# Kernel tuning notes

Hardware: AMD Instinct MI355X
Metric: run time of the kernel (lower is better)

Reference implementation:

```python
import jax, jax.numpy as jnp
import numpy as np

EPS = 1e-3  # BatchNorm eps from module

def _bn(x, g, b, m, v):
    # torch BatchNorm1d (eval): (x - mean) / sqrt(var + eps) * weight + bias
    return (x - m) * (g / jnp.sqrt(v + EPS)) + b

def setup_inputs() -> dict:
    key = jax.random.key(0)
    ks = jax.random.split(key, 16)
    N, Cin, Cout, S = 1_000_000, 16, 64, 20_000
    inputs = jax.random.normal(ks[0], (N, Cin), dtype=jnp.float32)
    unq_inv = jax.random.randint(ks[1], (N,), 0, S, dtype=jnp.int32)

    def bn_params(k, c):
        k1, k2, k3, k4 = jax.random.split(k, 4)
        return (1.0 + 0.01 * jax.random.normal(k1, (c,), jnp.float32),
                0.01 * jax.random.normal(k2, (c,), jnp.float32),
                0.01 * jax.random.normal(k3, (c,), jnp.float32),
                jax.random.uniform(k4, (c,), jnp.float32, 0.5, 1.5))

    W1 = 0.1 * jax.random.normal(ks[2], (Cin, Cout), jnp.float32)
    g1, b1, m1, v1 = bn_params(ks[3], Cout)
    W2a = 0.1 * jax.random.normal(ks[4], (Cin, 2 * Cout), jnp.float32)
    g2a, b2a, m2a, v2a = bn_params(ks[5], 2 * Cout)
    W2b = 0.1 * jax.random.normal(ks[6], (2 * Cout, Cout), jnp.float32)
    g2b, b2b, m2b, v2b = bn_params(ks[7], Cout)

    return dict(inputs=inputs, unq_inv=unq_inv, num_segments=S,
                W1=W1, g1=g1, b1=b1, m1=m1, v1=v1,
                W2a=W2a, g2a=g2a, b2a=b2a, m2a=m2a, v2a=v2a,
                W2b=W2b, g2b=b2b * 0 + g2b, b2b=b2b, m2b=m2b, v2b=v2b)

def reference(inputs, unq_inv, num_segments,
              W1, g1, b1, m1, v1,
              W2a, g2a, b2a, m2a, v2a,
              W2b, g2b, b2b, m2b, v2b):
    # branch 1: Linear -> BN -> ReLU
    x = jax.nn.relu(_bn(inputs @ W1, g1, b1, m1, v1))            # [N, C]
    # branch 2: Linear -> BN -> ReLU -> Linear -> BN -> ReLU
    h = jax.nn.relu(_bn(inputs @ W2a, g2a, b2a, m2a, v2a))       # [N, 2C]
    x2 = jax.nn.relu(_bn(h @ W2b, g2b, b2b, m2b, v2b))           # [N, C]

    # segment reductions over group ids
    x_max = jax.ops.segment_max(x, unq_inv, num_segments=num_segments)  # [S, C]
    x_max = jnp.maximum(x_max, 0.0)  # empty segments -> 0 (x >= 0 post-ReLU)
    group_sum = jax.ops.segment_sum(x, unq_inv, num_segments=num_segments)  # [S, C]
    max_pool = jnp.max(x2, axis=0)                                # [C], global pool
    max_pool = jnp.broadcast_to(max_pool[None, :], x_max.shape)   # [S, C]

    feat = jnp.concatenate((group_sum, x_max, max_pool), axis=1)  # [S, 3C]
    # channel shuffle with groups=3
    S_, C3 = feat.shape
    feat = feat.reshape(S_, 3, C3 // 3).transpose(0, 2, 1).reshape(S_, C3)
    return feat
```

## Files before the change

### kernel.cpp

```cpp
#include <hip/hip_runtime.h>

#define EPS 1e-3f

#define OFF_T2B    7168
#define OFF_MPP    7232
#define OFF_MPF    11328
#define OFF_CNT    11392
#define OFF_OFFS   31408
#define OFF_CUR    51424
#define OFF_INPS   71424

typedef short short8 __attribute__((ext_vector_type(8)));
typedef float f32x4 __attribute__((ext_vector_type(4)));

union U4 { unsigned u[4]; short8 s8; uint4 u4; };

__device__ inline unsigned short f2bf(float f) {
    unsigned u = __float_as_uint(f);
    return (unsigned short)((u + 0x7FFFu + ((u >> 16) & 1u)) >> 16);
}

__global__ __launch_bounds__(256) void init_k(
    const float* __restrict__ W1,
    const float* __restrict__ g1, const float* __restrict__ b1,
    const float* __restrict__ m1, const float* __restrict__ v1,
    const float* __restrict__ W2a,
    const float* __restrict__ g2a, const float* __restrict__ b2a,
    const float* __restrict__ m2a, const float* __restrict__ v2a,
    const float* __restrict__ W2b,
    const float* __restrict__ g2b, const float* __restrict__ b2b,
    const float* __restrict__ m2b, const float* __restrict__ v2b,
    unsigned short* __restrict__ wsu, float* __restrict__ wsf,
    const int* __restrict__ unq, int* __restrict__ cnt, int N)
{
    const int t = threadIdx.x;
    if (blockIdx.x == 0) {
        for (int i = t; i < 2048; i += 256) {
            int mt = i >> 9, lane = (i >> 3) & 63, j = i & 7;
            int c = lane & 15, g = lane >> 4;
            int k = g * 8 + j, ch = mt * 16 + c;
            float s = g1[ch] * rsqrtf(v1[ch] + EPS);
            float val = (k < 16) ? W1[k * 64 + ch] * s
                      : (k == 16 ? b1[ch] - m1[ch] * s : 0.f);
            wsu[i] = f2bf(val);
        }
        for (int i = t; i < 4096; i += 256) {
            int mt = i >> 9, lane = (i >> 3) & 63, j = i & 7;
            int c = lane & 15, g = lane >> 4;
            int k = g * 8 + j, ch = mt * 16 + c;
            float s = g2a[ch] * rsqrtf(v2a[ch] + EPS);
            float val = (k < 16) ? W2a[k * 128 + ch] * s
                      : (k == 16 ? b2a[ch] - m2a[ch] * s : 0.f);
            wsu[2048 + i] = f2bf(val);
        }
        for (int i = t; i < 8192; i += 256) {
            int f = i >> 9, lane = (i >> 3) & 63, j = i & 7;
            int mt = f >> 2, ks = f & 3;
            int c = lane & 15, g = lane >> 4;
            int k = ks * 32 + g * 8 + j, ch = mt * 16 + c;
            float s = g2b[ch] * rsqrtf(v2b[ch] + EPS);
            wsu[6144 + i] = f2bf(W2b[k * 64 + ch] * s);
        }
        if (t < 64) {
            float s = g2b[t] * rsqrtf(v2b[t] + EPS);
            wsf[OFF_T2B + t] = b2b[t] - m2b[t] * s;
        }
    } else {
        const int i = (blockIdx.x - 1) * 256 + t;
        if (i < N) atomicAdd(&cnt[unq[i]], 1);
    }
}

__global__ __launch_bounds__(1024) void scan_k(
    const int* __restrict__ cnt, int* __restrict__ offs,
    int* __restrict__ cur, int S)
{
    __shared__ int tot[1024];
    const int t = threadIdx.x;
    const int E = (S + 1023) >> 10;
    const int i0 = t * E;
    int run = 0;
    for (int j = 0; j < E; ++j) {
        const int i = i0 + j;
        run += (i < S) ? cnt[i] : 0;
    }
    tot[t] = run;
    __syncthreads();
    for (int d = 1; d < 1024; d <<= 1) {
        int x = (t >= d) ? tot[t - d] : 0;
        __syncthreads();
        tot[t] += x;
        __syncthreads();
    }
    int base = (t == 0) ? 0 : tot[t - 1];
    for (int j = 0; j < E; ++j) {
        const int i = i0 + j;
        if (i < S) {
            offs[i] = base;
            cur[i]  = base;
            base += cnt[i];
        }
    }
    if (t == 1023) offs[S] = tot[1023];
}

__device__ __forceinline__ void b2_tile(
    const U4& bf, bool act, const short8 (&w2a)[8],
    const char* __restrict__ w2bs, char* __restrict__ scr,
    float (&mp)[16], int lane, int c, int g)
{
    const f32x4 zero4 = {0.f, 0.f, 0.f, 0.f};
    __builtin_amdgcn_wave_barrier();
    #pragma unroll
    for (int mt = 0; mt < 8; ++mt) {
        f32x4 hT = __builtin_amdgcn_mfma_f32_16x16x32_bf16(w2a[mt], bf.s8, zero4, 0, 0, 0);
        float h0 = fmaxf(hT[0], 0.f), h1 = fmaxf(hT[1], 0.f);
        float h2 = fmaxf(hT[2], 0.f), h3 = fmaxf(hT[3], 0.f);
        unsigned lo, hi;
        asm("v_cvt_pk_bf16_f32 %0, %1, %2" : "=v"(lo) : "v"(h0), "v"(h1));
        asm("v_cvt_pk_bf16_f32 %0, %1, %2" : "=v"(hi) : "v"(h2), "v"(h3));
        const int gw = 2 * (mt & 1) + (g >> 1);
        *reinterpret_cast<uint2*>(
            &scr[(mt >> 1) * 1024 + (gw * 16 + c) * 16 + (g & 1) * 8])
            = make_uint2(lo, hi);
    }
    __builtin_amdgcn_wave_barrier();
    f32x4 y2t[4];
    #pragma unroll
    for (int mt = 0; mt < 4; ++mt) y2t[mt] = zero4;
    #pragma unroll
    for (int ks = 0; ks < 4; ++ks) {
        short8 hb = *reinterpret_cast<const short8*>(&scr[ks * 1024 + lane * 16]);
        #pragma unroll
        for (int mt = 0; mt < 4; ++mt) {
            short8 a = *reinterpret_cast<const short8*>(
                &w2bs[((mt * 4 + ks) * 64 + lane) * 16]);
            y2t[mt] = __builtin_amdgcn_mfma_f32_16x16x32_bf16(a, hb, y2t[mt], 0, 0, 0);
        }
    }
    #pragma unroll
    for (int mt = 0; mt < 4; ++mt) {
        #pragma unroll
        for (int r = 0; r < 4; ++r)
            mp[mt * 4 + r] = act ? fmaxf(mp[mt * 4 + r], y2t[mt][r]) : mp[mt * 4 + r];
    }
}

__global__ __launch_bounds__(256, 4) void br2_k(
    const float* __restrict__ inputs,
    const uint4* __restrict__ wsw,
    const float* __restrict__ wsf,
    float* __restrict__ mpp,
    int N)
{
    __shared__ __align__(16) char w2bs[16384];
    __shared__ __align__(16) char scrs[4][4096];
    __shared__ float mpb[64];

    const int tid  = threadIdx.x;
    const int wv   = tid >> 6;
    const int lane = tid & 63;
    const int c = lane & 15;
    const int g = lane >> 4;

    #pragma unroll
    for (int u = 0; u < 4; ++u)
        reinterpret_cast<uint4*>(w2bs)[u * 256 + tid] = wsw[768 + u * 256 + tid];
    if (tid < 64) mpb[tid] = 0.f;
    __syncthreads();

    short8 w2a[8];
    #pragma unroll
    for (int s = 0; s < 8; ++s) {
        U4 t; t.u4 = wsw[256 + s * 64 + lane]; w2a[s] = t.s8;
    }
    #pragma unroll
    for (int s = 0; s < 8; ++s) asm volatile("" : "+v"(w2a[s]));

    char* scr = scrs[wv];
    float mp[16];
    #pragma unroll
    for (int j = 0; j < 16; ++j) mp[j] = -3.0e38f;

    const long stride = (long)gridDim.x * 256;
    for (long base = (long)blockIdx.x * 256 + (long)wv * 64; base < N; base += stride) {
        const long nrem = (long)N - base;
        if (nrem >= 64) {
            float4 f0[4], f1[4];
            if (g < 2) {
                const float* ip = inputs + (base + c) * 16 + g * 8;
                #pragma unroll
                for (int ti = 0; ti < 4; ++ti) {
                    const float4* p = reinterpret_cast<const float4*>(ip + ti * 256);
                    f0[ti] = p[0]; f1[ti] = p[1];
                }
            }
            #pragma unroll
            for (int ti = 0; ti < 4; ++ti) {
                U4 bf;
                if (g < 2) {
                    asm("v_cvt_pk_bf16_f32 %0, %1, %2" : "=v"(bf.u[0]) : "v"(f0[ti].x), "v"(f0[ti].y));
                    asm("v_cvt_pk_bf16_f32 %0, %1, %2" : "=v"(bf.u[1]) : "v"(f0[ti].z), "v"(f0[ti].w));
                    asm("v_cvt_pk_bf16_f32 %0, %1, %2" : "=v"(bf.u[2]) : "v"(f1[ti].x), "v"(f1[ti].y));
                    asm("v_cvt_pk_bf16_f32 %0, %1, %2" : "=v"(bf.u[3]) : "v"(f1[ti].z), "v"(f1[ti].w));
                } else {
                    bf.u[0] = (g == 2) ? 0x00003F80u : 0u;
                    bf.u[1] = 0u; bf.u[2] = 0u; bf.u[3] = 0u;
                }
                b2_tile(bf, true, w2a, w2bs, scr, mp, lane, c, g);
            }
        } else {
            #pragma unroll
            for (int ti = 0; ti < 4; ++ti) {
                if ((long)ti * 16 >= nrem) break;
                const bool act = (long)(ti * 16 + c) < nrem;
                U4 bf;
                if (g < 2) {
                    const long row = act ? (base + ti * 16 + c) : (long)(N - 1);
                    const float4* p = reinterpret_cast<const float4*>(inputs + row * 16 + g * 8);
                    float4 q0 = p[0], q1 = p[1];
                    asm("v_cvt_pk_bf16_f32 %0, %1, %2" : "=v"(bf.u[0]) : "v"(q0.x), "v"(q0.y));
                    asm("v_cvt_pk_bf16_f32 %0, %1, %2" : "=v"(bf.u[1]) : "v"(q0.z), "v"(q0.w));
                    asm("v_cvt_pk_bf16_f32 %0, %1, %2" : "=v"(bf.u[2]) : "v"(q1.x), "v"(q1.y));
                    asm("v_cvt_pk_bf16_f32 %0, %1, %2" : "=v"(bf.u[3]) : "v"(q1.z), "v"(q1.w));
                    if (!act) { bf.u[0] = 0u; bf.u[1] = 0u; bf.u[2] = 0u; bf.u[3] = 0u; }
                } else {
                    bf.u[0] = (g == 2 && act) ? 0x00003F80u : 0u;
                    bf.u[1] = 0u; bf.u[2] = 0u; bf.u[3] = 0u;
                }
                b2_tile(bf, act, w2a, w2bs, scr, mp, lane, c, g);
            }
        }
    }

    #pragma unroll
    for (int j = 0; j < 16; ++j) {
        float x = mp[j];
        x = fmaxf(x, __shfl_xor(x, 1, 64));
        x = fmaxf(x, __shfl_xor(x, 2, 64));
        x = fmaxf(x, __shfl_xor(x, 4, 64));
        x = fmaxf(x, __shfl_xor(x, 8, 64));
        mp[j] = x;
    }
    if (c == 0) {
        #pragma unroll
        for (int mt = 0; mt < 4; ++mt)
            #pragma unroll
            for (int r = 0; r < 4; ++r) {
                const int ch = mt * 16 + g * 4 + r;
                const float v = fmaxf(mp[mt * 4 + r] + wsf[OFF_T2B + ch], 0.f);
                atomicMax(reinterpret_cast<int*>(&mpb[ch]), __float_as_int(v));
            }
    }
    __syncthreads();
    if (tid < 64)
        atomicMax(reinterpret_cast<int*>(mpp + (blockIdx.x & 63) * 64 + tid),
                  __float_as_int(mpb[tid]));
}

__global__ __launch_bounds__(256) void scat_k(
    const float* __restrict__ inputs,
    const int*   __restrict__ unq,
    int*         __restrict__ cur,
    uint4*       __restrict__ inpS,
    int N)
{
    const int i = blockIdx.x * 256 + threadIdx.x;
    if (i >= N) return;
    const int seg = unq[i];
    const int pos = atomicAdd(&cur[seg], 1);

    const float4* p = reinterpret_cast<const float4*>(inputs + (size_t)i * 16);
    float4 a0 = p[0], a1 = p[1], a2 = p[2], a3 = p[3];
    unsigned pk[8];
    asm("v_cvt_pk_bf16_f32 %0, %1, %2" : "=v"(pk[0]) : "v"(a0.x), "v"(a0.y));
    asm("v_cvt_pk_bf16_f32 %0, %1, %2" : "=v"(pk[1]) : "v"(a0.z), "v"(a0.w));
    asm("v_cvt_pk_bf16_f32 %0, %1, %2" : "=v"(pk[2]) : "v"(a1.x), "v"(a1.y));
    asm("v_cvt_pk_bf16_f32 %0, %1, %2" : "=v"(pk[3]) : "v"(a1.z), "v"(a1.w));
    asm("v_cvt_pk_bf16_f32 %0, %1, %2" : "=v"(pk[4]) : "v"(a2.x), "v"(a2.y));
    asm("v_cvt_pk_bf16_f32 %0, %1, %2" : "=v"(pk[5]) : "v"(a2.z), "v"(a2.w));
    asm("v_cvt_pk_bf16_f32 %0, %1, %2" : "=v"(pk[6]) : "v"(a3.x), "v"(a3.y));
    asm("v_cvt_pk_bf16_f32 %0, %1, %2" : "=v"(pk[7]) : "v"(a3.z), "v"(a3.w));

    inpS[(size_t)pos * 2]     = make_uint4(pk[0], pk[1], pk[2], pk[3]);
    inpS[(size_t)pos * 2 + 1] = make_uint4(pk[4], pk[5], pk[6], pk[7]);
}

__global__ __launch_bounds__(64) void fin_k(
    const float* __restrict__ mpp, float* __restrict__ mpf)
{
    const int t = threadIdx.x;
    float m = 0.f;
    #pragma unroll
    for (int s = 0; s < 64; ++s)
        m = fmaxf(m, mpp[s * 64 + t]);
    mpf[t] = m;
}

__global__ __launch_bounds__(256, 4) void seg1_k(
    const uint4* __restrict__ inpS,
    const int*   __restrict__ offs,
    const uint4* __restrict__ wsw,
    const float* __restrict__ mpf,
    float* __restrict__ out,
    int S)
{
    __shared__ float scr3[4][192];

    const int tid  = threadIdx.x;
    const int wv   = tid >> 6;
    const int lane = tid & 63;
    const int c = lane & 15;
    const int g = lane >> 4;

    short8 w1[4];
    #pragma unroll
    for (int mt = 0; mt < 4; ++mt) {
        U4 t; t.u4 = wsw[mt * 64 + lane]; w1[mt] = t.s8;
    }
    const float mpl = mpf[lane];
    float* sr = scr3[wv];
    const f32x4 zero4 = {0.f, 0.f, 0.f, 0.f};

    const int nw = gridDim.x * 4;
    for (int seg = blockIdx.x * 4 + wv; seg < S; seg += nw) {
        const int su    = __builtin_amdgcn_readfirstlane(seg);
        const int start = offs[su];
        const int end   = offs[su + 1];

        f32x4 as[4], am[4];
        #pragma unroll
        for (int mt = 0; mt < 4; ++mt) { as[mt] = zero4; am[mt] = zero4; }

        for (int base = start; base < end; base += 64) {
            const int nrem = end - base;
            #pragma unroll
            for (int ti = 0; ti < 4; ++ti) {
                if (ti * 16 >= nrem) break;
                const bool act = (ti * 16 + c) < nrem;

                U4 bf;
                if (g < 2) {
                    const int row = min(base + ti * 16 + c, end - 1);
                    uint4 q = inpS[(size_t)row * 2 + g];
                    bf.u[0] = act ? q.x : 0u;
                    bf.u[1] = act ? q.y : 0u;
                    bf.u[2] = act ? q.z : 0u;
                    bf.u[3] = act ? q.w : 0u;
                } else {
                    bf.u[0] = (g == 2 && act) ? 0x00003F80u : 0u;
                    bf.u[1] = 0u; bf.u[2] = 0u; bf.u[3] = 0u;
                }
                #pragma unroll
                for (int mt = 0; mt < 4; ++mt) {
                    f32x4 y1t = __builtin_amdgcn_mfma_f32_16x16x32_bf16(w1[mt], bf.s8, zero4, 0, 0, 0);
                    #pragma unroll
                    for (int r = 0; r < 4; ++r) {
                        float v = fmaxf(y1t[r], 0.f);
                        as[mt][r] += v;
                        am[mt][r]  = fmaxf(am[mt][r], v);
                    }
                }
            }
        }

        #pragma unroll
        for (int mt = 0; mt < 4; ++mt) {
            #pragma unroll
            for (int r = 0; r < 4; ++r) {
                float xs = as[mt][r], xm = am[mt][r];
                xs += __shfl_xor(xs, 1, 64);  xm = fmaxf(xm, __shfl_xor(xm, 1, 64));
                xs += __shfl_xor(xs, 2, 64);  xm = fmaxf(xm, __shfl_xor(xm, 2, 64));
                xs += __shfl_xor(xs, 4, 64);  xm = fmaxf(xm, __shfl_xor(xm, 4, 64));
                xs += __shfl_xor(xs, 8, 64);  xm = fmaxf(xm, __shfl_xor(xm, 8, 64));
                as[mt][r] = xs; am[mt][r] = xm;
            }
        }

        if (c == 0) {
            #pragma unroll
            for (int mt = 0; mt < 4; ++mt)
                #pragma unroll
                for (int r = 0; r < 4; ++r) {
                    const int ch = mt * 16 + g * 4 + r;
                    sr[ch * 3 + 0] = as[mt][r];
                    sr[ch * 3 + 1] = am[mt][r];
                }
        }
        sr[lane * 3 + 2] = mpl;
        __builtin_amdgcn_wave_barrier();
        asm volatile("s_waitcnt lgkmcnt(0)" ::: "memory");
        __builtin_amdgcn_sched_barrier(0);

        float* o = out + (size_t)seg * 192;
        #pragma unroll
        for (int p = 0; p < 3; ++p)
            o[p * 64 + lane] = sr[p * 64 + lane];
        __builtin_amdgcn_wave_barrier();
    }
}

extern "C" void kernel_launch(void* const* d_in, const int* in_sizes, int n_in,
                              void* d_out, int out_size, void* d_ws, size_t ws_size,
                              hipStream_t stream)
{
    const float* inputs = (const float*)d_in[0];
    const int*   unq    = (const int*)d_in[1];
    const float* W1  = (const float*)d_in[3];
    const float* g1  = (const float*)d_in[4];
    const float* b1  = (const float*)d_in[5];
    const float* m1  = (const float*)d_in[6];
    const float* v1  = (const float*)d_in[7];
    const float* W2a = (const float*)d_in[8];
    const float* g2a = (const float*)d_in[9];
    const float* b2a = (const float*)d_in[10];
    const float* m2a = (const float*)d_in[11];
    const float* v2a = (const float*)d_in[12];
    const float* W2b = (const float*)d_in[13];
    const float* g2b = (const float*)d_in[14];
    const float* b2b = (const float*)d_in[15];
    const float* m2b = (const float*)d_in[16];
    const float* v2b = (const float*)d_in[17];

    float* wsf = (float*)d_ws;
    float* out = (float*)d_out;
    const int N = in_sizes[0] / 16;
    const int S = out_size / 192;

    float* mpp  = wsf + OFF_MPP;
    float* mpf  = wsf + OFF_MPF;
    int*   cnt  = (int*)(wsf + OFF_CNT);
    int*   offs = (int*)(wsf + OFF_OFFS);
    int*   cur  = (int*)(wsf + OFF_CUR);
    uint4* inpS = (uint4*)(wsf + OFF_INPS);

    hipMemsetAsync(mpp, 0, (size_t)(OFF_CNT + 20016 - OFF_MPP) * sizeof(float), stream);

    init_k<<<1 + (N + 255) / 256, 256, 0, stream>>>(
        W1, g1, b1, m1, v1, W2a, g2a, b2a, m2a, v2a, W2b, g2b, b2b, m2b, v2b,
        (unsigned short*)d_ws, wsf, unq, cnt, N);

    br2_k<<<2048, 256, 0, stream>>>(inputs, (const uint4*)d_ws, wsf, mpp, N);

    scan_k<<<1, 1024, 0, stream>>>(cnt, offs, cur, S);

    scat_k<<<(N + 255) / 256, 256, 0, stream>>>(inputs, unq, cur, inpS, N);

    fin_k<<<1, 64, 0, stream>>>(mpp, mpf);

    seg1_k<<<2048, 256, 0, stream>>>(inpS, offs, (const uint4*)d_ws,
                                     mpf, out, S);
}
```

Before: 250.7 us.

## Fuse branch-2 max-pool with bf16 scatter and fold final max into segment kernel

Merges the branch-2 MLP/max-pool kernel with the scatter kernel, so the input rows are read once, converted to bf16, and both fed to the MFMA tiles and written to their sorted segment position. The final 64-way max-pool reduction kernel is removed, and each seg1 thread reduces the partial maxima itself. Two launches and one full extra read of the inputs are dropped, and grid sizes are halved. In exchange the fused loop always takes the guarded tail path, does per-row atomics inside the compute loop, and every seg1 thread issues 64 extra loads.

```diff
diff --git a/kernel.cpp b/kernel.cpp
--- a/kernel.cpp
+++ b/kernel.cpp
@@ -4,7 +4,6 @@
 
 #define OFF_T2B    7168
 #define OFF_MPP    7232
-#define OFF_MPF    11328
 #define OFF_CNT    11392
 #define OFF_OFFS   31408
 #define OFF_CUR    51424
@@ -146,8 +145,11 @@
     }
 }
 
-__global__ __launch_bounds__(256, 4) void br2_k(
+__global__ __launch_bounds__(256, 4) void brscat_k(
     const float* __restrict__ inputs,
+    const int*   __restrict__ unq,
+    int*         __restrict__ cur,
+    uint4*       __restrict__ inpS,
     const uint4* __restrict__ wsw,
     const float* __restrict__ wsf,
     float* __restrict__ mpp,
@@ -185,51 +187,36 @@
     const long stride = (long)gridDim.x * 256;
     for (long base = (long)blockIdx.x * 256 + (long)wv * 64; base < N; base += stride) {
         const long nrem = (long)N - base;
-        if (nrem >= 64) {
-            float4 f0[4], f1[4];
+
+        const long ip = base + lane;
+        int pos = 0;
+        if (ip < (long)N) pos = atomicAdd(&cur[unq[ip]], 1);
+
+        #pragma unroll
+        for (int ti = 0; ti < 4; ++ti) {
+            if ((long)ti * 16 >= nrem) break;
+            const bool act = (long)(ti * 16 + c) < nrem;
+
+            U4 bf;
             if (g < 2) {
-                const float* ip = inputs + (base + c) * 16 + g * 8;
-                #pragma unroll
-                for (int ti = 0; ti < 4; ++ti) {
-                    const float4* p = reinterpret_cast<const float4*>(ip + ti * 256);
-                    f0[ti] = p[0]; f1[ti] = p[1];
-                }
+                const long row = act ? (base + ti * 16 + c) : (long)(N - 1);
+                const float4* p = reinterpret_cast<const float4*>(inputs + row * 16 + g * 8);
+                float4 q0 = p[0], q1 = p[1];
+                asm("v_cvt_pk_bf16_f32 %0, %1, %2" : "=v"(bf.u[0]) : "v"(q0.x), "v"(q0.y));
+                asm("v_cvt_pk_bf16_f32 %0, %1, %2" : "=v"(bf.u[1]) : "v"(q0.z), "v"(q0.w));
+                asm("v_cvt_pk_bf16_f32 %0, %1, %2" : "=v"(bf.u[2]) : "v"(q1.x), "v"(q1.y));
+                asm("v_cvt_pk_bf16_f32 %0, %1, %2" : "=v"(bf.u[3]) : "v"(q1.z), "v"(q1.w));
+                if (!act) { bf.u[0] = 0u; bf.u[1] = 0u; bf.u[2] = 0u; bf.u[3] = 0u; }
+            } else {
+                bf.u[0] = (g == 2 && act) ? 0x00003F80u : 0u;
+                bf.u[1] = 0u; bf.u[2] = 0u; bf.u[3] = 0u;
             }
-            #pragma unroll
-            for (int ti = 0; ti < 4; ++ti) {
-                U4 bf;
-                if (g < 2) {
-                    asm("v_cvt_pk_bf16_f32 %0, %1, %2" : "=v"(bf.u[0]) : "v"(f0[ti].x), "v"(f0[ti].y));
-                    asm("v_cvt_pk_bf16_f32 %0, %1, %2" : "=v"(bf.u[1]) : "v"(f0[ti].z), "v"(f0[ti].w));
-                    asm("v_cvt_pk_bf16_f32 %0, %1, %2" : "=v"(bf.u[2]) : "v"(f1[ti].x), "v"(f1[ti].y));
-                    asm("v_cvt_pk_bf16_f32 %0, %1, %2" : "=v"(bf.u[3]) : "v"(f1[ti].z), "v"(f1[ti].w));
-                } else {
-                    bf.u[0] = (g == 2) ? 0x00003F80u : 0u;
-                    bf.u[1] = 0u; bf.u[2] = 0u; bf.u[3] = 0u;
-                }
-                b2_tile(bf, true, w2a, w2bs, scr, mp, lane, c, g);
-            }
-        } else {
-            #pragma unroll
-            for (int ti = 0; ti < 4; ++ti) {
-                if ((long)ti * 16 >= nrem) break;
-                const bool act = (long)(ti * 16 + c) < nrem;
-                U4 bf;
-                if (g < 2) {
-                    const long row = act ? (base + ti * 16 + c) : (long)(N - 1);
-                    const float4* p = reinterpret_cast<const float4*>(inputs + row * 16 + g * 8);
-                    float4 q0 = p[0], q1 = p[1];
-                    asm("v_cvt_pk_bf16_f32 %0, %1, %2" : "=v"(bf.u[0]) : "v"(q0.x), "v"(q0.y));
-                    asm("v_cvt_pk_bf16_f32 %0, %1, %2" : "=v"(bf.u[1]) : "v"(q0.z), "v"(q0.w));
-                    asm("v_cvt_pk_bf16_f32 %0, %1, %2" : "=v"(bf.u[2]) : "v"(q1.x), "v"(q1.y));
-                    asm("v_cvt_pk_bf16_f32 %0, %1, %2" : "=v"(bf.u[3]) : "v"(q1.z), "v"(q1.w));
-                    if (!act) { bf.u[0] = 0u; bf.u[1] = 0u; bf.u[2] = 0u; bf.u[3] = 0u; }
-                } else {
-                    bf.u[0] = (g == 2 && act) ? 0x00003F80u : 0u;
-                    bf.u[1] = 0u; bf.u[2] = 0u; bf.u[3] = 0u;
-                }
-                b2_tile(bf, act, w2a, w2bs, scr, mp, lane, c, g);
-            }
+
+            const int posc = __shfl(pos, ti * 16 + c, 64);
+            if (g < 2 && act)
+                inpS[(size_t)posc * 2 + g] = bf.u4;
+
+            b2_tile(bf, act, w2a, w2bs, scr, mp, lane, c, g);
         }
     }
 
@@ -258,50 +245,11 @@
                   __float_as_int(mpb[tid]));
 }
 
-__global__ __launch_bounds__(256) void scat_k(
-    const float* __restrict__ inputs,
-    const int*   __restrict__ unq,
-    int*         __restrict__ cur,
-    uint4*       __restrict__ inpS,
-    int N)
-{
-    const int i = blockIdx.x * 256 + threadIdx.x;
-    if (i >= N) return;
-    const int seg = unq[i];
-    const int pos = atomicAdd(&cur[seg], 1);
-
-    const float4* p = reinterpret_cast<const float4*>(inputs + (size_t)i * 16);
-    float4 a0 = p[0], a1 = p[1], a2 = p[2], a3 = p[3];
-    unsigned pk[8];
-    asm("v_cvt_pk_bf16_f32 %0, %1, %2" : "=v"(pk[0]) : "v"(a0.x), "v"(a0.y));
-    asm("v_cvt_pk_bf16_f32 %0, %1, %2" : "=v"(pk[1]) : "v"(a0.z), "v"(a0.w));
-    asm("v_cvt_pk_bf16_f32 %0, %1, %2" : "=v"(pk[2]) : "v"(a1.x), "v"(a1.y));
-    asm("v_cvt_pk_bf16_f32 %0, %1, %2" : "=v"(pk[3]) : "v"(a1.z), "v"(a1.w));
-    asm("v_cvt_pk_bf16_f32 %0, %1, %2" : "=v"(pk[4]) : "v"(a2.x), "v"(a2.y));
-    asm("v_cvt_pk_bf16_f32 %0, %1, %2" : "=v"(pk[5]) : "v"(a2.z), "v"(a2.w));
-    asm("v_cvt_pk_bf16_f32 %0, %1, %2" : "=v"(pk[6]) : "v"(a3.x), "v"(a3.y));
-    asm("v_cvt_pk_bf16_f32 %0, %1, %2" : "=v"(pk[7]) : "v"(a3.z), "v"(a3.w));
-
-    inpS[(size_t)pos * 2]     = make_uint4(pk[0], pk[1], pk[2], pk[3]);
-    inpS[(size_t)pos * 2 + 1] = make_uint4(pk[4], pk[5], pk[6], pk[7]);
-}
-
-__global__ __launch_bounds__(64) void fin_k(
-    const float* __restrict__ mpp, float* __restrict__ mpf)
-{
-    const int t = threadIdx.x;
-    float m = 0.f;
-    #pragma unroll
-    for (int s = 0; s < 64; ++s)
-        m = fmaxf(m, mpp[s * 64 + t]);
-    mpf[t] = m;
-}
-
 __global__ __launch_bounds__(256, 4) void seg1_k(
     const uint4* __restrict__ inpS,
     const int*   __restrict__ offs,
     const uint4* __restrict__ wsw,
-    const float* __restrict__ mpf,
+    const float* __restrict__ mpp,
     float* __restrict__ out,
     int S)
 {
@@ -318,7 +266,11 @@
     for (int mt = 0; mt < 4; ++mt) {
         U4 t; t.u4 = wsw[mt * 64 + lane]; w1[mt] = t.s8;
     }
-    const float mpl = mpf[lane];
+    float mpl = 0.f;
+    #pragma unroll
+    for (int s = 0; s < 64; ++s)
+        mpl = fmaxf(mpl, mpp[s * 64 + lane]);
+
     float* sr = scr3[wv];
     const f32x4 zero4 = {0.f, 0.f, 0.f, 0.f};
 
@@ -428,7 +380,6 @@
     const int S = out_size / 192;
 
     float* mpp  = wsf + OFF_MPP;
-    float* mpf  = wsf + OFF_MPF;
     int*   cnt  = (int*)(wsf + OFF_CNT);
     int*   offs = (int*)(wsf + OFF_OFFS);
     int*   cur  = (int*)(wsf + OFF_CUR);
@@ -440,14 +391,11 @@
         W1, g1, b1, m1, v1, W2a, g2a, b2a, m2a, v2a, W2b, g2b, b2b, m2b, v2b,
         (unsigned short*)d_ws, wsf, unq, cnt, N);
 
-    br2_k<<<2048, 256, 0, stream>>>(inputs, (const uint4*)d_ws, wsf, mpp, N);
-
     scan_k<<<1, 1024, 0, stream>>>(cnt, offs, cur, S);
 
-    scat_k<<<(N + 255) / 256, 256, 0, stream>>>(inputs, unq, cur, inpS, N);
-
-    fin_k<<<1, 64, 0, stream>>>(mpp, mpf);
-
-    seg1_k<<<2048, 256, 0, stream>>>(inpS, offs, (const uint4*)d_ws,
-                                     mpf, out, S);
-}
+    brscat_k<<<1024, 256, 0, stream>>>(inputs, unq, cur, inpS,
+                                       (const uint4*)d_ws, wsf, mpp, N);
+
+    seg1_k<<<1024, 256, 0, stream>>>(inpS, offs, (const uint4*)d_ws,
+                                     mpp, out, S);
+}
```

After: 213.4 us. 14.9% less time.
